# Performance work log

Hardware: AMD Instinct MI355X
Metric: run time of the kernel (lower is better)

Reference implementation:

```python
import jax, jax.numpy as jnp
import numpy as np

E = 384      # n_embed
H = 6        # n_head
HS = E // H  # head_size = 64
B = 64
T = 256      # == block_size
FF = 4 * E


def _layernorm(x, g, b, eps=1e-5):
    m = x.mean(-1, keepdims=True)
    v = ((x - m) ** 2).mean(-1, keepdims=True)
    return (x - m) / jnp.sqrt(v + eps) * g + b


def _mha(q_in, k_in, v_in, wq, bq, wk, bk, wv, bv, pw, pb):
    # Faithful to source: scale uses q_in's last dim (n_embed=384), NOT head_size,
    # and the causal tril mask is applied even in cross-attention.
    scale = q_in.shape[-1] ** -0.5
    q = jnp.einsum('bte,hes->bhts', q_in, wq) + bq[None, :, None, :]  # [B,H,T1,HS]
    k = jnp.einsum('bue,hes->bhus', k_in, wk) + bk[None, :, None, :]  # [B,H,T2,HS]
    v = jnp.einsum('bue,hes->bhus', v_in, wv) + bv[None, :, None, :]
    wei = jnp.einsum('bhts,bhus->bhtu', q, k) * scale                 # [B,H,T1,T2]
    T1, T2 = q_in.shape[1], k_in.shape[1]
    mask = jnp.tril(jnp.ones((T1, T2), dtype=bool))
    wei = jnp.where(mask[None, None], wei, -jnp.inf)
    wei = jax.nn.softmax(wei, axis=-1)
    out = jnp.einsum('bhtu,bhus->bths', wei, v)                       # [B,T1,H,HS]
    out = out.reshape(out.shape[0], out.shape[1], -1)                 # concat heads
    return out @ pw + pb


def setup_inputs() -> dict:
    key = jax.random.key(0)
    ks = jax.random.split(key, 32)
    s = 0.02
    d = {
        'encode_output': jax.random.normal(ks[0], (B, T, E), jnp.float32),
        'x': jax.random.normal(ks[1], (B, T, E), jnp.float32),
    }
    i = 2
    for p in ('sa1', 'sa2'):
        d[p + '_wq'] = jax.random.normal(ks[i], (H, E, HS), jnp.float32) * s; i += 1
        d[p + '_bq'] = jnp.zeros((H, HS), jnp.float32)
        d[p + '_wk'] = jax.random.normal(ks[i], (H, E, HS), jnp.float32) * s; i += 1
        d[p + '_bk'] = jnp.zeros((H, HS), jnp.float32)
        d[p + '_wv'] = jax.random.normal(ks[i], (H, E, HS), jnp.float32) * s; i += 1
        d[p + '_bv'] = jnp.zeros((H, HS), jnp.float32)
        d[p + '_pw'] = jax.random.normal(ks[i], (E, E), jnp.float32) * s; i += 1
        d[p + '_pb'] = jnp.zeros((E,), jnp.float32)
    d['ff_w1'] = jax.random.normal(ks[i], (E, FF), jnp.float32) * s; i += 1
    d['ff_b1'] = jnp.zeros((FF,), jnp.float32)
    d['ff_w2'] = jax.random.normal(ks[i], (FF, E), jnp.float32) * s; i += 1
    d['ff_b2'] = jnp.zeros((E,), jnp.float32)
    for n in ('ln1', 'ln2', 'ln3'):
        d[n + '_g'] = jnp.ones((E,), jnp.float32)
        d[n + '_b'] = jnp.zeros((E,), jnp.float32)
    return d


def reference(encode_output, x,
              sa1_wq, sa1_bq, sa1_wk, sa1_bk, sa1_wv, sa1_bv, sa1_pw, sa1_pb,
              sa2_wq, sa2_bq, sa2_wk, sa2_bk, sa2_wv, sa2_bv, sa2_pw, sa2_pb,
              ff_w1, ff_b1, ff_w2, ff_b2,
              ln1_g, ln1_b, ln2_g, ln2_b, ln3_g, ln3_b):
    # masked self-attention + add&norm
    a1 = _mha(x, x, x, sa1_wq, sa1_bq, sa1_wk, sa1_bk, sa1_wv, sa1_bv, sa1_pw, sa1_pb)
    o1 = _layernorm(x + a1, ln1_g, ln1_b)
    # cross-attention (q=o1, k=v=encode_output) + add&norm
    a2 = _mha(o1, encode_output, encode_output,
              sa2_wq, sa2_bq, sa2_wk, sa2_bk, sa2_wv, sa2_bv, sa2_pw, sa2_pb)
    o2 = _layernorm(o1 + a2, ln2_g, ln2_b)
    # FFN + add&norm
    f = jax.nn.relu(o2 @ ff_w1 + ff_b1) @ ff_w2 + ff_b2
    return _layernorm(o2 + f, ln3_g, ln3_b)
```

## Files before the change

### kernel.cpp

```cpp
#include <hip/hip_runtime.h>

typedef __attribute__((ext_vector_type(8))) short bf16x8;
typedef __attribute__((ext_vector_type(4))) float f32x4;
typedef __attribute__((ext_vector_type(4))) int i32x4;

__device__ __forceinline__ float b2f(ushort b) {
    union { unsigned int u; float f; } x;
    x.u = ((unsigned int)b) << 16;
    return x.f;
}
__device__ __forceinline__ ushort f2b(float f) {
    union { float f; unsigned int u; } x;
    x.f = f;
    unsigned int r = x.u + 0x7fffu + ((x.u >> 16) & 1u);
    return (ushort)(r >> 16);
}
__device__ __forceinline__ int4 pack8(float4 a, float4 b) {
    union { int4 v; ushort u[8]; } r;
    r.u[0] = f2b(a.x); r.u[1] = f2b(a.y); r.u[2] = f2b(a.z); r.u[3] = f2b(a.w);
    r.u[4] = f2b(b.x); r.u[5] = f2b(b.y); r.u[6] = f2b(b.z); r.u[7] = f2b(b.w);
    return r.v;
}
__device__ __forceinline__ i32x4 add_resb(i32x4 cs, i32x4 rs) {
    const ushort* c = (const ushort*)&cs; const ushort* r = (const ushort*)&rs;
    union { i32x4 v; ushort u[8]; } o;
#pragma unroll
    for (int j = 0; j < 8; j++) o.u[j] = f2b(b2f(c[j]) + b2f(r[j]));
    return o.v;
}
__device__ __forceinline__ i32x4 add_resf(i32x4 cs, f32x4 r0, f32x4 r1) {
    const ushort* c = (const ushort*)&cs;
    union { i32x4 v; ushort u[8]; } o;
#pragma unroll
    for (int j = 0; j < 4; j++) o.u[j] = f2b(b2f(c[j]) + r0[j]);
#pragma unroll
    for (int j = 0; j < 4; j++) o.u[4 + j] = f2b(b2f(c[4 + j]) + r1[j]);
    return o.v;
}

__device__ __forceinline__ void gll16(const ushort* g, ushort* l) {
    __builtin_amdgcn_global_load_lds(
        (__attribute__((address_space(1))) void*)(g),
        (__attribute__((address_space(3))) void*)(l), 16, 0, 0);
}

template<int MI>
__global__ __launch_bounds__(256) void gemm_bs(
    const ushort* __restrict__ A, const ushort* __restrict__ Bt,
    ushort* __restrict__ C, const float* __restrict__ bias,
    const ushort* __restrict__ resb, const float* __restrict__ resf,
    int N, int K, int relu)
{
    __shared__ __align__(16) ushort sm[8704];
    constexpr int CHUNK = MI * 64;
    constexpr int PERX  = (16384 / CHUNK) / 8;
    const int tid  = threadIdx.x;
    const int wave = tid >> 6, lane = tid & 63;
    const int qd = lane >> 4, lc = lane & 15;
    const int id = blockIdx.x, xcd = id & 7, sub = id >> 3;
    const int mc = sub % PERX, ct = sub / PERX;
    const int row0 = (xcd * PERX + mc) * CHUNK;
    const int col0 = ct * 64;

    f32x4 acc[MI][4];
#pragma unroll
    for (int i = 0; i < MI; i++)
#pragma unroll
        for (int j = 0; j < 4; j++) acc[i][j] = 0.0f;

    const ushort* Aw = A + (size_t)(row0 + wave * MI * 16 + lc) * K + qd * 8;
    const ushort* Bw = Bt + (size_t)(col0 + wave * 16 + (lane >> 2)) * K + (lane & 3) * 8;
    ushort* Bsw = &sm[wave * 512];

    const int NKC = K >> 7;
    for (int kc = 0; kc < NKC; ++kc) {
        if (kc) __syncthreads();
#pragma unroll
        for (int j = 0; j < 4; j++)
            gll16(Bw + kc * 128 + j * 32, Bsw + j * 2048);
        __syncthreads();

        const ushort* Akc = Aw + kc * 128;
#pragma unroll
        for (int kk = 0; kk < 4; ++kk) {
            bf16x8 af[MI];
#pragma unroll
            for (int mi = 0; mi < MI; mi++)
                af[mi] = *(const bf16x8*)(Akc + (size_t)mi * 16 * K + kk * 32);
            bf16x8 bfr[4];
#pragma unroll
            for (int ni = 0; ni < 4; ni++)
                bfr[ni] = *(const bf16x8*)&sm[kk * 2048 + (ni * 16 + lc) * 32 + qd * 8];
            __builtin_amdgcn_s_setprio(1);
#pragma unroll
            for (int mi = 0; mi < MI; mi++)
#pragma unroll
                for (int ni = 0; ni < 4; ni++)
                    acc[mi][ni] = __builtin_amdgcn_mfma_f32_16x16x32_bf16(
                        af[mi], bfr[ni], acc[mi][ni], 0, 0, 0);
            __builtin_amdgcn_s_setprio(0);
        }
    }

    __syncthreads();
    ushort* Csw = &sm[wave * MI * 16 * 68];
#pragma unroll
    for (int mi = 0; mi < MI; mi++)
#pragma unroll
        for (int r = 0; r < 4; r++) {
            int lr = mi * 16 + qd * 4 + r;
#pragma unroll
            for (int ni = 0; ni < 4; ni++) {
                float v = acc[mi][ni][r];
                if (bias) v += bias[col0 + ni * 16 + lc];
                if (relu) v = fmaxf(v, 0.0f);
                Csw[lr * 68 + ni * 16 + lc] = f2b(v);
            }
        }
    asm volatile("s_waitcnt lgkmcnt(0)" ::: "memory");
    const int rowW = row0 + wave * MI * 16;
#pragma unroll
    for (int p = 0; p < MI * 2; p++) {
        int lr = p * 8 + (lane >> 3), cc = (lane & 7) * 8;
        size_t base = (size_t)(rowW + lr) * N + col0 + cc;
        i32x4 d = *(const i32x4*)&Csw[lr * 68 + cc];
        if (resb) d = add_resb(d, __builtin_nontemporal_load((const i32x4*)&resb[base]));
        else if (resf) d = add_resf(d,
                __builtin_nontemporal_load((const f32x4*)&resf[base]),
                __builtin_nontemporal_load((const f32x4*)&resf[base + 4]));
        __builtin_nontemporal_store(d, (i32x4*)&C[base]);
    }
}

__global__ __launch_bounds__(256) void gemm_bs_dual(
    const ushort* __restrict__ A1, const ushort* __restrict__ B1t,
    ushort* __restrict__ C1, const float* __restrict__ bias1, int N1,
    const ushort* __restrict__ A2, const ushort* __restrict__ B2t,
    ushort* __restrict__ C2, const float* __restrict__ bias2, int N2,
    int split)
{
    __shared__ __align__(16) ushort sm[8704];
    const int K = 384;
    const int tid  = threadIdx.x;
    const int wave = tid >> 6, lane = tid & 63;
    const int qd = lane >> 4, lc = lane & 15;
    const int id = blockIdx.x, xcd = id & 7, sub = id >> 3;
    const int mc = sub & 15, ct = sub >> 4;
    const int row0 = (xcd * 16 + mc) * 128;
    const bool first = ct < split;
    const ushort* A  = first ? A1 : A2;
    const ushort* Bt = first ? B1t : B2t;
    ushort* C        = first ? C1 : C2;
    const float* bias = first ? bias1 : bias2;
    const int N      = first ? N1 : N2;
    const int col0   = (first ? ct : ct - split) * 64;

    f32x4 acc[2][4];
#pragma unroll
    for (int i = 0; i < 2; i++)
#pragma unroll
        for (int j = 0; j < 4; j++) acc[i][j] = 0.0f;

    const ushort* Aw = A + (size_t)(row0 + wave * 32 + lc) * K + qd * 8;
    const ushort* Bw = Bt + (size_t)(col0 + wave * 16 + (lane >> 2)) * K + (lane & 3) * 8;
    ushort* Bsw = &sm[wave * 512];

    for (int kc = 0; kc < 3; ++kc) {
        if (kc) __syncthreads();
#pragma unroll
        for (int j = 0; j < 4; j++)
            gll16(Bw + kc * 128 + j * 32, Bsw + j * 2048);
        __syncthreads();

        const ushort* Akc = Aw + kc * 128;
#pragma unroll
        for (int kk = 0; kk < 4; ++kk) {
            bf16x8 af[2];
#pragma unroll
            for (int mi = 0; mi < 2; mi++)
                af[mi] = *(const bf16x8*)(Akc + (size_t)mi * 16 * K + kk * 32);
            bf16x8 bfr[4];
#pragma unroll
            for (int ni = 0; ni < 4; ni++)
                bfr[ni] = *(const bf16x8*)&sm[kk * 2048 + (ni * 16 + lc) * 32 + qd * 8];
            __builtin_amdgcn_s_setprio(1);
#pragma unroll
            for (int mi = 0; mi < 2; mi++)
#pragma unroll
                for (int ni = 0; ni < 4; ni++)
                    acc[mi][ni] = __builtin_amdgcn_mfma_f32_16x16x32_bf16(
                        af[mi], bfr[ni], acc[mi][ni], 0, 0, 0);
            __builtin_amdgcn_s_setprio(0);
        }
    }

    __syncthreads();
    ushort* Csw = &sm[wave * 32 * 68];
#pragma unroll
    for (int mi = 0; mi < 2; mi++)
#pragma unroll
        for (int r = 0; r < 4; r++) {
            int lr = mi * 16 + qd * 4 + r;
#pragma unroll
            for (int ni = 0; ni < 4; ni++)
                Csw[lr * 68 + ni * 16 + lc] = f2b(acc[mi][ni][r] + bias[col0 + ni * 16 + lc]);
        }
    asm volatile("s_waitcnt lgkmcnt(0)" ::: "memory");
    const int rowW = row0 + wave * 32;
#pragma unroll
    for (int p = 0; p < 4; p++) {
        int lr = p * 8 + (lane >> 3), cc = (lane & 7) * 8;
        size_t base = (size_t)(rowW + lr) * N + col0 + cc;
        __builtin_nontemporal_store(*(const i32x4*)&Csw[lr * 68 + cc], (i32x4*)&C[base]);
    }
}

__global__ __launch_bounds__(256) void attn(
    const ushort* __restrict__ q, int qstr,
    const ushort* __restrict__ k, int kstr,
    const ushort* __restrict__ v, int vstr,
    ushort* __restrict__ out)
{
    __shared__ __align__(16) ushort Qs[64 * 72];
    __shared__ __align__(16) ushort Kc[64 * 72];
    __shared__ __align__(16) ushort Vc[64 * 72];
    __shared__ __align__(16) ushort Ps[64 * 264];

    const int tid = threadIdx.x;
    const int wave = tid >> 6, lane = tid & 63;
    const int qd = lane >> 4, lc = lane & 15;
    const int b = blockIdx.z, h = blockIdx.y, t0 = blockIdx.x * 64;
    const int hc = h * 64;
    const float scale = 0.051031036307982884f;

    {
        int r = tid >> 2, c = (tid & 3) * 16;
        int4 q0 = *(const int4*)&q[(size_t)(b * 256 + t0 + r) * qstr + hc + c];
        int4 q1 = *(const int4*)&q[(size_t)(b * 256 + t0 + r) * qstr + hc + c + 8];
        *(int4*)&Qs[r * 72 + c] = q0;
        *(int4*)&Qs[r * 72 + c + 8] = q1;
    }

    f32x4 accS[16];
#pragma unroll
    for (int j = 0; j < 16; j++) accS[j] = 0.0f;

    for (int uc = 0; uc < 4; uc++) {
        int r = tid >> 2, c = (tid & 3) * 16;
        int4 k0v = *(const int4*)&k[(size_t)(b * 256 + uc * 64 + r) * kstr + hc + c];
        int4 k1v = *(const int4*)&k[(size_t)(b * 256 + uc * 64 + r) * kstr + hc + c + 8];
        __syncthreads();
        *(int4*)&Kc[r * 72 + c] = k0v;
        *(int4*)&Kc[r * 72 + c + 8] = k1v;
        __syncthreads();
#pragma unroll
        for (int s0 = 0; s0 < 64; s0 += 32) {
            bf16x8 a = *(const bf16x8*)&Qs[(wave * 16 + lc) * 72 + s0 + qd * 8];
#pragma unroll
            for (int ni = 0; ni < 4; ni++) {
                bf16x8 bb = *(const bf16x8*)&Kc[(ni * 16 + lc) * 72 + s0 + qd * 8];
                accS[uc * 4 + ni] =
                    __builtin_amdgcn_mfma_f32_16x16x32_bf16(a, bb, accS[uc * 4 + ni], 0, 0, 0);
            }
        }
    }

#pragma unroll
    for (int rr = 0; rr < 4; rr++) {
        int t = t0 + wave * 16 + qd * 4 + rr;
        float pv[16];
        float mx = -3.0e38f;
#pragma unroll
        for (int j = 0; j < 16; j++) {
            int u = (j >> 2) * 64 + (j & 3) * 16 + lc;
            float s = accS[j][rr] * scale;
            s = (u <= t) ? s : -3.0e38f;
            pv[j] = s;
            mx = fmaxf(mx, s);
        }
#pragma unroll
        for (int m = 1; m < 16; m <<= 1) mx = fmaxf(mx, __shfl_xor(mx, m, 16));
        float sum = 0.0f;
#pragma unroll
        for (int j = 0; j < 16; j++) { float p = __expf(pv[j] - mx); pv[j] = p; sum += p; }
#pragma unroll
        for (int m = 1; m < 16; m <<= 1) sum += __shfl_xor(sum, m, 16);
        float inv = 1.0f / sum;
#pragma unroll
        for (int j = 0; j < 16; j++) {
            int u = (j >> 2) * 64 + (j & 3) * 16 + lc;
            Ps[(wave * 16 + qd * 4 + rr) * 264 + u] = f2b(pv[j] * inv);
        }
    }

    f32x4 accO[4];
#pragma unroll
    for (int j = 0; j < 4; j++) accO[j] = 0.0f;
    for (int uc = 0; uc < 4; uc++) {
        int r = tid >> 2, s0 = (tid & 3) * 16;
        int4 v0 = *(const int4*)&v[(size_t)(b * 256 + uc * 64 + r) * vstr + hc + s0];
        int4 v1 = *(const int4*)&v[(size_t)(b * 256 + uc * 64 + r) * vstr + hc + s0 + 8];
        __syncthreads();
        {
            const ushort* t0p = (const ushort*)&v0;
            const ushort* t1p = (const ushort*)&v1;
#pragma unroll
            for (int j = 0; j < 8; j++) Vc[(s0 + j) * 72 + r] = t0p[j];
#pragma unroll
            for (int j = 0; j < 8; j++) Vc[(s0 + 8 + j) * 72 + r] = t1p[j];
        }
        __syncthreads();
#pragma unroll
        for (int u0 = 0; u0 < 64; u0 += 32) {
            bf16x8 a = *(const bf16x8*)&Ps[(wave * 16 + lc) * 264 + uc * 64 + u0 + qd * 8];
#pragma unroll
            for (int ni = 0; ni < 4; ni++) {
                bf16x8 bb = *(const bf16x8*)&Vc[(ni * 16 + lc) * 72 + u0 + qd * 8];
                accO[ni] = __builtin_amdgcn_mfma_f32_16x16x32_bf16(a, bb, accO[ni], 0, 0, 0);
            }
        }
    }

#pragma unroll
    for (int ni = 0; ni < 4; ni++)
#pragma unroll
        for (int rr = 0; rr < 4; rr++) {
            int t = t0 + wave * 16 + qd * 4 + rr;
            out[(size_t)(b * 256 + t) * 384 + hc + ni * 16 + lc] = f2b(accO[ni][rr]);
        }
}

__global__ __launch_bounds__(256) void lnorm(
    const ushort* __restrict__ in, const float* __restrict__ g,
    const float* __restrict__ be, ushort* __restrict__ outb,
    float* __restrict__ outf)
{
    const int wave = threadIdx.x >> 6, lane = threadIdx.x & 63;
    const int row = blockIdx.x * 4 + wave;
    const ushort* r = in + (size_t)row * 384;
    float x[6], s1 = 0.0f, s2 = 0.0f;
#pragma unroll
    for (int j = 0; j < 6; j++) {
        x[j] = b2f(r[j * 64 + lane]);
        s1 += x[j]; s2 += x[j] * x[j];
    }
#pragma unroll
    for (int m = 1; m < 64; m <<= 1) {
        s1 += __shfl_xor(s1, m, 64);
        s2 += __shfl_xor(s2, m, 64);
    }
    float mean = s1 * (1.0f / 384.0f);
    float var  = s2 * (1.0f / 384.0f) - mean * mean;
    float rstd = rsqrtf(var + 1e-5f);
#pragma unroll
    for (int j = 0; j < 6; j++) {
        float y = (x[j] - mean) * rstd * g[j * 64 + lane] + be[j * 64 + lane];
        if (outb) outb[(size_t)row * 384 + j * 64 + lane] = f2b(y);
        if (outf) outf[(size_t)row * 384 + j * 64 + lane] = y;
    }
}

__device__ __forceinline__ void dev_cvt(const float* in, ushort* out, int blk) {
    size_t i = ((size_t)blk * 256 + threadIdx.x) * 8;
    float4 a = *(const float4*)(in + i);
    float4 b = *(const float4*)(in + i + 4);
    *(int4*)(out + i) = pack8(a, b);
}
__device__ __forceinline__ void dev_transp(const float* in, ushort* out,
                                           int R, int C, int bx, int by,
                                           float (*t)[33]) {
    const int tx = threadIdx.x & 31, ty = threadIdx.x >> 5;
    const int c0 = bx * 32, r0 = by * 32;
#pragma unroll
    for (int i = 0; i < 32; i += 8)
        t[ty + i][tx] = in[(size_t)(r0 + ty + i) * C + c0 + tx];
    __syncthreads();
#pragma unroll
    for (int i = 0; i < 32; i += 8)
        out[(size_t)(c0 + ty + i) * R + r0 + tx] = f2b(t[tx][ty + i]);
}
__device__ __forceinline__ void dev_packqkv(const float* wq, const float* wk,
                                            const float* wv, ushort* Wt,
                                            int blk, float (*t)[33]) {
    const int tx = threadIdx.x & 31, ty = threadIdx.x >> 5;
    const int bx = blk % 12, by = (blk / 12) % 2, bz = blk / 24;
    const int e0 = bx * 32, s0 = by * 32;
    const int seg = bz / 6, h = bz - seg * 6;
    const float* w = (seg == 0) ? wq : (seg == 1) ? wk : wv;
    const float* wh = w + (size_t)h * 384 * 64;
#pragma unroll
    for (int i = 0; i < 32; i += 8)
        t[ty + i][tx] = wh[(size_t)(e0 + ty + i) * 64 + s0 + tx];
    __syncthreads();
    const int nbase = seg * 384 + h * 64 + s0;
#pragma unroll
    for (int i = 0; i < 32; i += 8)
        Wt[(size_t)(nbase + ty + i) * 384 + e0 + tx] = f2b(t[tx][ty + i]);
}

__global__ __launch_bounds__(256) void prep_all(
    const float* __restrict__ x, ushort* __restrict__ xb,
    const float* __restrict__ enc, ushort* __restrict__ encb,
    const float* __restrict__ s1wq, const float* __restrict__ s1wk,
    const float* __restrict__ s1wv, ushort* __restrict__ W1,
    const float* __restrict__ s2wq, const float* __restrict__ s2wk,
    const float* __restrict__ s2wv, ushort* __restrict__ W2,
    const float* __restrict__ s1pw, ushort* __restrict__ pw1t,
    const float* __restrict__ s2pw, ushort* __restrict__ pw2t,
    const float* __restrict__ fw1, ushort* __restrict__ w1t,
    const float* __restrict__ fw2, ushort* __restrict__ w2t,
    const float* __restrict__ s1bq, const float* __restrict__ s1bk,
    const float* __restrict__ s1bv, const float* __restrict__ s2bq,
    const float* __restrict__ s2bk, const float* __restrict__ s2bv,
    float* __restrict__ bias1, float* __restrict__ bias2)
{
    __shared__ float t[32][33];
    int blk = blockIdx.x;
    if (blk < 3072) { dev_cvt(x, xb, blk); return; }
    blk -= 3072;
    if (blk < 3072) { dev_cvt(enc, encb, blk); return; }
    blk -= 3072;
    if (blk < 432) { dev_packqkv(s1wq, s1wk, s1wv, W1, blk, t); return; }
    blk -= 432;
    if (blk < 432) { dev_packqkv(s2wq, s2wk, s2wv, W2, blk, t); return; }
    blk -= 432;
    if (blk < 144) { dev_transp(s1pw, pw1t, 384, 384, blk % 12, blk / 12, t); return; }
    blk -= 144;
    if (blk < 144) { dev_transp(s2pw, pw2t, 384, 384, blk % 12, blk / 12, t); return; }
    blk -= 144;
    if (blk < 576) { dev_transp(fw1, w1t, 384, 1536, blk % 48, blk / 48, t); return; }
    blk -= 576;
    if (blk < 576) { dev_transp(fw2, w2t, 1536, 384, blk % 12, blk / 12, t); return; }
    blk -= 576;
    int i = blk * 256 + threadIdx.x;
    if (i >= 2304) return;
    int grp = i / 1152, r = i - grp * 1152;
    int seg = r / 384, nn = r - seg * 384;
    const float* src = grp == 0 ? (seg == 0 ? s1bq : seg == 1 ? s1bk : s1bv)
                                : (seg == 0 ? s2bq : seg == 1 ? s2bk : s2bv);
    (grp == 0 ? bias1 : bias2)[r] = src[nn];
}

extern "C" void kernel_launch(void* const* d_in, const int* in_sizes, int n_in,
                              void* d_out, int out_size, void* d_ws, size_t ws_size,
                              hipStream_t stream)
{
    const float* enc = (const float*)d_in[0];
    const float* x   = (const float*)d_in[1];
    const float* s1wq = (const float*)d_in[2];  const float* s1bq = (const float*)d_in[3];
    const float* s1wk = (const float*)d_in[4];  const float* s1bk = (const float*)d_in[5];
    const float* s1wv = (const float*)d_in[6];  const float* s1bv = (const float*)d_in[7];
    const float* s1pw = (const float*)d_in[8];  const float* s1pb = (const float*)d_in[9];
    const float* s2wq = (const float*)d_in[10]; const float* s2bq = (const float*)d_in[11];
    const float* s2wk = (const float*)d_in[12]; const float* s2bk = (const float*)d_in[13];
    const float* s2wv = (const float*)d_in[14]; const float* s2bv = (const float*)d_in[15];
    const float* s2pw = (const float*)d_in[16]; const float* s2pb = (const float*)d_in[17];
    const float* fw1 = (const float*)d_in[18];  const float* fb1 = (const float*)d_in[19];
    const float* fw2 = (const float*)d_in[20];  const float* fb2 = (const float*)d_in[21];
    const float* g1 = (const float*)d_in[22];   const float* be1 = (const float*)d_in[23];
    const float* g2 = (const float*)d_in[24];   const float* be2 = (const float*)d_in[25];
    const float* g3 = (const float*)d_in[26];   const float* be3 = (const float*)d_in[27];

    if (ws_size < 80216064u) return;

    ushort* wsp = (ushort*)d_ws;
    ushort* qkv1 = wsp;
    ushort* q2   = wsp;
    ushort* kv2  = wsp + 6291456;
    ushort* h1   = wsp;
    ushort* att  = wsp + 18874368;
    ushort* xb   = wsp + 18874368;
    ushort* tmp  = wsp + 25165824;
    ushort* o1b  = wsp + 31457280;
    ushort* W1   = wsp + 37748736;
    ushort* W2   = W1 + 442368;
    ushort* pw1t = W2 + 442368;
    ushort* pw2t = pw1t + 147456;
    ushort* w1t  = pw2t + 147456;
    ushort* w2t  = w1t + 589824;

    ushort* encb = (ushort*)d_out;
    ushort* o2b  = (ushort*)d_out;
    float* bias1 = (float*)((ushort*)d_out + 6291456);
    float* bias2 = bias1 + 1152;

    prep_all<<<dim3(8457), dim3(256), 0, stream>>>(
        x, xb, enc, encb,
        s1wq, s1wk, s1wv, W1, s2wq, s2wk, s2wv, W2,
        s1pw, pw1t, s2pw, pw2t, fw1, w1t, fw2, w2t,
        s1bq, s1bk, s1bv, s2bq, s2bk, s2bv, bias1, bias2);

    gemm_bs<2><<<dim3(2304), dim3(256), 0, stream>>>(
        xb, W1, qkv1, bias1, nullptr, nullptr, 1152, 384, 0);
    attn<<<dim3(4, 6, 64), dim3(256), 0, stream>>>(
        qkv1, 1152, qkv1 + 384, 1152, qkv1 + 768, 1152, att);
    gemm_bs<2><<<dim3(768), dim3(256), 0, stream>>>(
        att, pw1t, tmp, s1pb, nullptr, x, 384, 384, 0);
    lnorm<<<dim3(4096), dim3(256), 0, stream>>>(tmp, g1, be1, o1b, nullptr);

    gemm_bs_dual<<<dim3(2304), dim3(256), 0, stream>>>(
        o1b, W2, q2, bias2, 384,
        encb, W2 + 147456, kv2, bias2 + 384, 768, 6);
    attn<<<dim3(4, 6, 64), dim3(256), 0, stream>>>(
        q2, 384, kv2, 768, kv2 + 384, 768, att);
    gemm_bs<2><<<dim3(768), dim3(256), 0, stream>>>(
        att, pw2t, tmp, s2pb, o1b, nullptr, 384, 384, 0);
    lnorm<<<dim3(4096), dim3(256), 0, stream>>>(tmp, g2, be2, o2b, nullptr);

    gemm_bs<2><<<dim3(3072), dim3(256), 0, stream>>>(
        o2b, w1t, h1, fb1, nullptr, nullptr, 1536, 384, 1);
    gemm_bs<2><<<dim3(768), dim3(256), 0, stream>>>(
        h1, w2t, tmp, fb2, o2b, nullptr, 384, 1536, 0);
    lnorm<<<dim3(4096), dim3(256), 0, stream>>>(tmp, g3, be3, nullptr, (float*)d_out);
}
```

Baseline: 464.2 us.

## Fuse projection GEMMs with residual add and LayerNorm into one kernel

Adds a gemm_ln kernel in which each wave computes a full 16x384 output row strip, so the residual add and LayerNorm can be applied in registers. This replaces three GEMM+lnorm launch pairs and removes the tmp buffer round trip through memory. The attention kernel also now aliases its shared-memory buffers (Ps overlapping Qs/Kc) behind an added barrier, which cuts its LDS footprint. In exchange, the new GEMM reads A and B straight from global memory with no LDS tiling, launches only 256 blocks with a large accumulator per thread, and writes its outputs with scalar stores. That may lower occupancy and make the FFN down-projection (K=1536) slower.

```diff
diff --git a/kernel.cpp b/kernel.cpp
--- a/kernel.cpp
+++ b/kernel.cpp
@@ -215,16 +215,95 @@
     }
 }
 
+__global__ __launch_bounds__(256) void gemm_ln(
+    const ushort* __restrict__ A, const ushort* __restrict__ Bt, int K,
+    const float* __restrict__ bias,
+    const ushort* __restrict__ resb, const float* __restrict__ resf,
+    const float* __restrict__ g, const float* __restrict__ be,
+    ushort* __restrict__ outb, float* __restrict__ outf)
+{
+    const int tid  = threadIdx.x;
+    const int wave = tid >> 6, lane = tid & 63;
+    const int qd = lane >> 4, lc = lane & 15;
+    const int id = blockIdx.x, xcd = id & 7, sub = id >> 3;
+    const int row0 = (xcd * 32 + sub) * 64;
+    const int rw0 = row0 + wave * 16;
+
+    f32x4 acc[24];
+#pragma unroll
+    for (int i = 0; i < 24; i++) acc[i] = 0.0f;
+
+    const ushort* Ap = A + (size_t)(rw0 + lc) * K + qd * 8;
+    const ushort* Bp = Bt + (size_t)lc * K + qd * 8;
+
+    const int K32 = K >> 5;
+    for (int kk = 0; kk < K32; ++kk) {
+        bf16x8 af = *(const bf16x8*)(Ap + kk * 32);
+#pragma unroll
+        for (int ni = 0; ni < 24; ni++) {
+            bf16x8 bfr = *(const bf16x8*)(Bp + (size_t)ni * 16 * K + kk * 32);
+            acc[ni] = __builtin_amdgcn_mfma_f32_16x16x32_bf16(af, bfr, acc[ni], 0, 0, 0);
+        }
+    }
+
+#pragma unroll
+    for (int ni = 0; ni < 24; ni++) {
+        float bc = bias[ni * 16 + lc];
+#pragma unroll
+        for (int r = 0; r < 4; r++) {
+            size_t idx = (size_t)(rw0 + qd * 4 + r) * 384 + ni * 16 + lc;
+            float rv = resb ? b2f(resb[idx]) : resf[idx];
+            acc[ni][r] += bc + rv;
+        }
+    }
+
+    float s1[4] = {0.f, 0.f, 0.f, 0.f}, s2[4] = {0.f, 0.f, 0.f, 0.f};
+#pragma unroll
+    for (int ni = 0; ni < 24; ni++)
+#pragma unroll
+        for (int r = 0; r < 4; r++) {
+            s1[r] += acc[ni][r];
+            s2[r] += acc[ni][r] * acc[ni][r];
+        }
+#pragma unroll
+    for (int m = 1; m < 16; m <<= 1)
+#pragma unroll
+        for (int r = 0; r < 4; r++) {
+            s1[r] += __shfl_xor(s1[r], m, 16);
+            s2[r] += __shfl_xor(s2[r], m, 16);
+        }
+    float mean[4], rstd[4];
+#pragma unroll
+    for (int r = 0; r < 4; r++) {
+        mean[r] = s1[r] * (1.0f / 384.0f);
+        float var = s2[r] * (1.0f / 384.0f) - mean[r] * mean[r];
+        rstd[r] = rsqrtf(var + 1e-5f);
+    }
+
+#pragma unroll
+    for (int ni = 0; ni < 24; ni++) {
+        float gg = g[ni * 16 + lc], bb = be[ni * 16 + lc];
+#pragma unroll
+        for (int r = 0; r < 4; r++) {
+            float y = (acc[ni][r] - mean[r]) * rstd[r] * gg + bb;
+            size_t idx = (size_t)(rw0 + qd * 4 + r) * 384 + ni * 16 + lc;
+            if (outb) outb[idx] = f2b(y);
+            if (outf) outf[idx] = y;
+        }
+    }
+}
+
 __global__ __launch_bounds__(256) void attn(
     const ushort* __restrict__ q, int qstr,
     const ushort* __restrict__ k, int kstr,
     const ushort* __restrict__ v, int vstr,
     ushort* __restrict__ out)
 {
-    __shared__ __align__(16) ushort Qs[64 * 72];
-    __shared__ __align__(16) ushort Kc[64 * 72];
-    __shared__ __align__(16) ushort Vc[64 * 72];
-    __shared__ __align__(16) ushort Ps[64 * 264];
+    __shared__ __align__(16) ushort sm[21504];
+    ushort* Qs = sm;
+    ushort* Kc = sm + 4608;
+    ushort* Ps = sm;
+    ushort* Vc = sm + 16896;
 
     const int tid = threadIdx.x;
     const int wave = tid >> 6, lane = tid & 63;
@@ -264,6 +343,8 @@
             }
         }
     }
+
+    __syncthreads();
 
 #pragma unroll
     for (int rr = 0; rr < 4; rr++) {
@@ -328,36 +409,6 @@
             int t = t0 + wave * 16 + qd * 4 + rr;
             out[(size_t)(b * 256 + t) * 384 + hc + ni * 16 + lc] = f2b(accO[ni][rr]);
         }
-}
-
-__global__ __launch_bounds__(256) void lnorm(
-    const ushort* __restrict__ in, const float* __restrict__ g,
-    const float* __restrict__ be, ushort* __restrict__ outb,
-    float* __restrict__ outf)
-{
-    const int wave = threadIdx.x >> 6, lane = threadIdx.x & 63;
-    const int row = blockIdx.x * 4 + wave;
-    const ushort* r = in + (size_t)row * 384;
-    float x[6], s1 = 0.0f, s2 = 0.0f;
-#pragma unroll
-    for (int j = 0; j < 6; j++) {
-        x[j] = b2f(r[j * 64 + lane]);
-        s1 += x[j]; s2 += x[j] * x[j];
-    }
-#pragma unroll
-    for (int m = 1; m < 64; m <<= 1) {
-        s1 += __shfl_xor(s1, m, 64);
-        s2 += __shfl_xor(s2, m, 64);
-    }
-    float mean = s1 * (1.0f / 384.0f);
-    float var  = s2 * (1.0f / 384.0f) - mean * mean;
-    float rstd = rsqrtf(var + 1e-5f);
-#pragma unroll
-    for (int j = 0; j < 6; j++) {
-        float y = (x[j] - mean) * rstd * g[j * 64 + lane] + be[j * 64 + lane];
-        if (outb) outb[(size_t)row * 384 + j * 64 + lane] = f2b(y);
-        if (outf) outf[(size_t)row * 384 + j * 64 + lane] = y;
-    }
 }
 
 __device__ __forceinline__ void dev_cvt(const float* in, ushort* out, int blk) {
@@ -470,7 +521,7 @@
     ushort* h1   = wsp;
     ushort* att  = wsp + 18874368;
     ushort* xb   = wsp + 18874368;
-    ushort* tmp  = wsp + 25165824;
+    ushort* o2b  = wsp + 25165824;
     ushort* o1b  = wsp + 31457280;
     ushort* W1   = wsp + 37748736;
     ushort* W2   = W1 + 442368;
@@ -480,7 +531,6 @@
     ushort* w2t  = w1t + 589824;
 
     ushort* encb = (ushort*)d_out;
-    ushort* o2b  = (ushort*)d_out;
     float* bias1 = (float*)((ushort*)d_out + 6291456);
     float* bias2 = bias1 + 1152;
 
@@ -494,22 +544,19 @@
         xb, W1, qkv1, bias1, nullptr, nullptr, 1152, 384, 0);
     attn<<<dim3(4, 6, 64), dim3(256), 0, stream>>>(
         qkv1, 1152, qkv1 + 384, 1152, qkv1 + 768, 1152, att);
-    gemm_bs<2><<<dim3(768), dim3(256), 0, stream>>>(
-        att, pw1t, tmp, s1pb, nullptr, x, 384, 384, 0);
-    lnorm<<<dim3(4096), dim3(256), 0, stream>>>(tmp, g1, be1, o1b, nullptr);
+    gemm_ln<<<dim3(256), dim3(256), 0, stream>>>(
+        att, pw1t, 384, s1pb, nullptr, x, g1, be1, o1b, nullptr);
 
     gemm_bs_dual<<<dim3(2304), dim3(256), 0, stream>>>(
         o1b, W2, q2, bias2, 384,
         encb, W2 + 147456, kv2, bias2 + 384, 768, 6);
     attn<<<dim3(4, 6, 64), dim3(256), 0, stream>>>(
         q2, 384, kv2, 768, kv2 + 384, 768, att);
-    gemm_bs<2><<<dim3(768), dim3(256), 0, stream>>>(
-        att, pw2t, tmp, s2pb, o1b, nullptr, 384, 384, 0);
-    lnorm<<<dim3(4096), dim3(256), 0, stream>>>(tmp, g2, be2, o2b, nullptr);
+    gemm_ln<<<dim3(256), dim3(256), 0, stream>>>(
+        att, pw2t, 384, s2pb, o1b, nullptr, g2, be2, o2b, nullptr);
 
     gemm_bs<2><<<dim3(3072), dim3(256), 0, stream>>>(
         o2b, w1t, h1, fb1, nullptr, nullptr, 1536, 384, 1);
-    gemm_bs<2><<<dim3(768), dim3(256), 0, stream>>>(
-        h1, w2t, tmp, fb2, o2b, nullptr, 384, 1536, 0);
-    lnorm<<<dim3(4096), dim3(256), 0, stream>>>(tmp, g3, be3, nullptr, (float*)d_out);
-}
+    gemm_ln<<<dim3(256), dim3(256), 0, stream>>>(
+        h1, w2t, 1536, fb2, o2b, nullptr, g3, be3, nullptr, (float*)d_out);
+}
```

New measurement: 607.7 us. 30.9% more time.
